# Optimization experiments

Measured on AMD Instinct MI355X. Metric: run time of the kernel, lower is better.

Reference implementation:

```python
import jax, jax.numpy as jnp
import numpy as np

N_NODES = 100000
N_HYPEREDGES = 30000
N_INC = 300000
IN_CH = 128
HID = 256
OUT_CH = 128
EPS = 1e-5


def setup_inputs() -> dict:
    key = jax.random.key(0)
    ks = jax.random.split(key, 14)
    x = jax.random.normal(ks[0], (N_NODES, IN_CH), jnp.float32)
    node_idx = jax.random.randint(ks[1], (N_INC,), 0, N_NODES)
    he_idx = jax.random.randint(ks[2], (N_INC,), 0, N_HYPEREDGES)
    edge = jnp.stack([node_idx, he_idx], axis=0)  # [2, N_INC]
    s1 = 1.0 / np.sqrt(IN_CH)
    s2 = 1.0 / np.sqrt(HID)
    return {
        "x": x,
        "edge": edge,
        "W1": jax.random.normal(ks[3], (IN_CH, HID), jnp.float32) * s1,
        "b1": jnp.zeros((HID,), jnp.float32),
        "g1": jnp.ones((HID,), jnp.float32),
        "be1": jnp.zeros((HID,), jnp.float32),
        "W2": jax.random.normal(ks[4], (HID, HID), jnp.float32) * s2,
        "b2": jnp.zeros((HID,), jnp.float32),
        "g2": jnp.ones((HID,), jnp.float32),
        "be2": jnp.zeros((HID,), jnp.float32),
        "W3": jax.random.normal(ks[5], (HID, OUT_CH), jnp.float32) * s2,
        "b3": jnp.zeros((OUT_CH,), jnp.float32),
    }


def _hconv(x, node_idx, he_idx, W, b):
    # PyG HypergraphConv (no attention, unit hyperedge weights):
    # X' = D^{-1} H B^{-1} H^T (X @ W) + b
    x = x @ W  # [N, F]
    ones = jnp.ones((node_idx.shape[0],), x.dtype)
    d = jax.ops.segment_sum(ones, node_idx, num_segments=N_NODES)       # node degree
    bd = jax.ops.segment_sum(ones, he_idx, num_segments=N_HYPEREDGES)  # hyperedge degree
    Dinv = jnp.where(d > 0, 1.0 / jnp.maximum(d, 1.0), 0.0)
    Binv = jnp.where(bd > 0, 1.0 / jnp.maximum(bd, 1.0), 0.0)
    # node -> hyperedge aggregation, scaled by B^{-1}
    he = jax.ops.segment_sum(x[node_idx], he_idx, num_segments=N_HYPEREDGES) * Binv[:, None]
    # hyperedge -> node aggregation, scaled by D^{-1}
    out = jax.ops.segment_sum(he[he_idx], node_idx, num_segments=N_NODES) * Dinv[:, None]
    return out + b


def _bn(x, g, be):
    # BatchNorm1d, training mode (batch statistics over nodes)
    m = x.mean(axis=0)
    v = x.var(axis=0)
    return (x - m) * jax.lax.rsqrt(v + EPS) * g + be


def reference(x, edge, W1, b1, g1, be1, W2, b2, g2, be2, W3, b3):
    node_idx = edge[0]
    he_idx = edge[1]
    h = _bn(jax.nn.relu(_hconv(x, node_idx, he_idx, W1, b1)), g1, be1)
    h = _bn(jax.nn.relu(_hconv(h, node_idx, he_idx, W2, b2)), g2, be2)
    h = jax.nn.relu(_hconv(h, node_idx, he_idx, W3, b3))
    return h
```

## Files before the change

kernel.cpp:

```cpp
#include <hip/hip_runtime.h>

#define N_NODES 100000
#define N_HE    30000
#define N_INC   300000
#define HEPAD   30080
#define NREP    16

typedef short  short8  __attribute__((ext_vector_type(8)));
typedef float  floatx4 __attribute__((ext_vector_type(4)));
typedef unsigned int uintx4 __attribute__((ext_vector_type(4)));

__device__ inline unsigned short f2bf(float f) {
  unsigned int u = __float_as_uint(f);
  u = (u + 0x7fff + ((u >> 16) & 1)) >> 16;
  return (unsigned short)u;
}
__device__ inline unsigned int pack2(float lo, float hi) {
  return (unsigned int)f2bf(lo) | ((unsigned int)f2bf(hi) << 16);
}
__device__ inline void acc8(uint4 rv, float* a) {
  unsigned int u;
  u = rv.x; a[0] += __uint_as_float(u << 16); a[1] += __uint_as_float(u & 0xffff0000u);
  u = rv.y; a[2] += __uint_as_float(u << 16); a[3] += __uint_as_float(u & 0xffff0000u);
  u = rv.z; a[4] += __uint_as_float(u << 16); a[5] += __uint_as_float(u & 0xffff0000u);
  u = rv.w; a[6] += __uint_as_float(u << 16); a[7] += __uint_as_float(u & 0xffff0000u);
}

struct R4 { uint4 r[4]; };
struct R8 { uint4 r[8]; };

__device__ inline void load4(const unsigned short* __restrict__ base, const int* e,
                             int F, int c0, R4& o) {
#pragma unroll
  for (int k = 0; k < 4; k++)
    o.r[k] = *(const uint4*)(base + (size_t)e[k] * F + c0);
}
__device__ inline void accm4(const R4& o, int d, float* a) {
  if (d > 0) acc8(o.r[0], a);
  if (d > 1) acc8(o.r[1], a);
  if (d > 2) acc8(o.r[2], a);
  if (d > 3) acc8(o.r[3], a);
}
__device__ inline void load8(const unsigned short* __restrict__ base, const int* e,
                             int F, int c0, R8& o) {
#pragma unroll
  for (int k = 0; k < 8; k++)
    o.r[k] = *(const uint4*)(base + (size_t)e[k] * F + c0);
}
__device__ inline void accm8(const R8& o, int d, float* a) {
  acc8(o.r[0], a);
  if (d > 1) acc8(o.r[1], a);
  if (d > 2) acc8(o.r[2], a);
  if (d > 3) acc8(o.r[3], a);
  if (d > 4) acc8(o.r[4], a);
  if (d > 5) acc8(o.r[5], a);
  if (d > 6) acc8(o.r[6], a);
  if (d > 7) acc8(o.r[7], a);
}

__device__ inline void gather8p(const unsigned short* __restrict__ base,
                                const int* __restrict__ idx, int beg, int end,
                                int F, int c0, float* a) {
  if (beg >= end) return;
  int e[8];
#pragma unroll
  for (int k = 0; k < 8; k++) e[k] = idx[min(beg + k, end - 1)];
  for (int j = beg; j < end; j += 8) {
    R8 r;
    load8(base, e, F, c0, r);
    int jn = j + 8;
    if (jn < end) {
#pragma unroll
      for (int k = 0; k < 8; k++) e[k] = idx[min(jn + k, end - 1)];
    }
    accm8(r, end - j, a);
  }
}


__global__ void count_kernel(const int* __restrict__ nidx, const int* __restrict__ hidx,
                             int* __restrict__ node_cnt, int* __restrict__ he_cnt) {
  int i = blockIdx.x * blockDim.x + threadIdx.x;
  if (i < N_INC) {
    atomicAdd(&node_cnt[nidx[i]], 1);
    atomicAdd(&he_cnt[hidx[i]], 1);
  }
}

__global__ void scan1(const int* __restrict__ cnt, int* __restrict__ incl,
                      int* __restrict__ bsums, int n) {
  __shared__ int tmp[1024];
  int tid = threadIdx.x;
  int i = blockIdx.x * 1024 + tid;
  tmp[tid] = (i < n) ? cnt[i] : 0;
  __syncthreads();
  for (int off = 1; off < 1024; off <<= 1) {
    int t = (tid >= off) ? tmp[tid - off] : 0;
    __syncthreads();
    tmp[tid] += t;
    __syncthreads();
  }
  if (i < n) incl[i] = tmp[tid];
  if (tid == 1023) bsums[blockIdx.x] = tmp[1023];
}

__global__ void scan2(int* __restrict__ bsums, int nb) {
  if (threadIdx.x == 0 && blockIdx.x == 0) {
    int run = 0;
    for (int b = 0; b < nb; b++) { int v = bsums[b]; bsums[b] = run; run += v; }
  }
}

__global__ void scan3(const int* __restrict__ cnt, const int* __restrict__ incl,
                      const int* __restrict__ bsums, int* __restrict__ ptr,
                      int* __restrict__ fill, int n) {
  int i = blockIdx.x * 1024 + threadIdx.x;
  if (i < n) {
    int e = incl[i] - cnt[i] + bsums[blockIdx.x];
    ptr[i] = e;
    fill[i] = e;
    if (i == n - 1) ptr[n] = incl[i] + bsums[blockIdx.x];
  }
}

__global__ void fill_kernel(const int* __restrict__ nidx, const int* __restrict__ hidx,
                            int* __restrict__ node_fill, int* __restrict__ he_fill,
                            int* __restrict__ node_hes, int* __restrict__ he_nodes) {
  int i = blockIdx.x * blockDim.x + threadIdx.x;
  if (i < N_INC) {
    int nn = nidx[i], hh = hidx[i];
    int p1 = atomicAdd(&node_fill[nn], 1);
    node_hes[p1] = hh;
    int p2 = atomicAdd(&he_fill[hh], 1);
    he_nodes[p2] = nn;
  }
}


__global__ void convert_x(const float* __restrict__ x, unsigned short* __restrict__ xb) {
  int i = blockIdx.x * 256 + threadIdx.x;
  if (i >= N_NODES * 16) return;
  const float4* p = (const float4*)x + (size_t)i * 2;
  float4 a = p[0], b = p[1];
  uint4 o;
  o.x = pack2(a.x, a.y); o.y = pack2(a.z, a.w);
  o.z = pack2(b.x, b.y); o.w = pack2(b.z, b.w);
  *(uint4*)(xb + (size_t)i * 8) = o;
}

__global__ __launch_bounds__(256) void fold_w(
    const float* __restrict__ W, const float* __restrict__ gsum,
    const float* __restrict__ gss, const float* __restrict__ g,
    const float* __restrict__ be, unsigned short* __restrict__ WT,
    float* __restrict__ cvec, int K, int N, float invN) {
  int n = blockIdx.y * 256 + threadIdx.x;
  if (n >= N) return;
  int k0 = blockIdx.x * 16;
  float c = 0.f;
  unsigned short loc[16];
#pragma unroll
  for (int i = 0; i < 16; i++) {
    int k = k0 + i;
    float w = W[(size_t)k * N + n];
    float s = 1.f, t = 0.f;
    if (gsum) {
      float ms = 0.f, vs = 0.f;
#pragma unroll
      for (int r = 0; r < NREP; r++) { ms += gsum[r * 256 + k]; vs += gss[r * 256 + k]; }
      float m = ms * invN;
      float v = vs * invN - m * m;
      s = g[k] * rsqrtf(v + 1e-5f);
      t = be[k] - m * s;
    }
    loc[i] = f2bf(w * s);
    c += t * w;
  }
  *(uint4*)(WT + (size_t)n * K + k0)     = *(const uint4*)&loc[0];
  *(uint4*)(WT + (size_t)n * K + k0 + 8) = *(const uint4*)&loc[8];
  atomicAdd(cvec + n, c);
}


__global__ __launch_bounds__(256) void gemm_mfma(
    const unsigned short* __restrict__ A, const unsigned short* __restrict__ BT,
    unsigned short* __restrict__ C, int K, int N) {
  __shared__ unsigned short As[128 * 32];
  __shared__ unsigned short Bs[128 * 32];
  const int tid  = threadIdx.x;
  const int w    = tid >> 6, lane = tid & 63;
  const int wm   = w & 1,  wn   = w >> 1;
  const int bm   = blockIdx.x * 128, bn = blockIdx.y * 128;
  const int quad = lane >> 4, r16 = lane & 15;

  floatx4 acc[4][4] = {};

  const int srow = (lane >> 2);
  const int scol = (lane & 3) * 8;

  for (int kb = 0; kb < K; kb += 32) {
#pragma unroll
    for (int i = 0; i < 2; i++) {
      const int row = (w * 2 + i) * 16 + srow;
      const unsigned short* ga = A  + (size_t)(bm + row) * K + kb + scol;
      const unsigned short* gb = BT + (size_t)(bn + row) * K + kb + scol;
      __builtin_amdgcn_global_load_lds(
          (const __attribute__((address_space(1))) void*)ga,
          (__attribute__((address_space(3))) void*)(&As[(w * 2 + i) * 512]), 16, 0, 0);
      __builtin_amdgcn_global_load_lds(
          (const __attribute__((address_space(1))) void*)gb,
          (__attribute__((address_space(3))) void*)(&Bs[(w * 2 + i) * 512]), 16, 0, 0);
    }
    __syncthreads();
    short8 af[4], bfr[4];
#pragma unroll
    for (int t = 0; t < 4; t++) {
      af[t]  = *(const short8*)&As[(wm * 64 + t * 16 + r16) * 32 + quad * 8];
      bfr[t] = *(const short8*)&Bs[(wn * 64 + t * 16 + r16) * 32 + quad * 8];
    }
#pragma unroll
    for (int mi = 0; mi < 4; mi++)
#pragma unroll
      for (int ni = 0; ni < 4; ni++)
        acc[mi][ni] = __builtin_amdgcn_mfma_f32_16x16x32_bf16(af[mi], bfr[ni], acc[mi][ni], 0, 0, 0);
    __syncthreads();
  }
#pragma unroll
  for (int mi = 0; mi < 4; mi++)
#pragma unroll
    for (int ni = 0; ni < 4; ni++)
#pragma unroll
      for (int rr = 0; rr < 4; rr++) {
        int gm = bm + wm * 64 + mi * 16 + quad * 4 + rr;
        int gn = bn + wn * 64 + ni * 16 + r16;
        C[(size_t)gm * N + gn] = f2bf(acc[mi][ni][rr]);
      }
}


__global__ __launch_bounds__(256) void agg_he(
    const unsigned short* __restrict__ src, const int* __restrict__ ptr,
    const int* __restrict__ idx, unsigned short* __restrict__ dst,
    int F, int shift, int nSeg) {
  int seg = blockIdx.x * (256 >> shift) + (threadIdx.x >> shift);
  if (seg >= nSeg) return;
  int l = threadIdx.x & ((1 << shift) - 1);
  int c0 = l * 8;
  int beg = ptr[seg], end = ptr[seg + 1];
  float a[8] = {};
  gather8p(src, idx, beg, end, F, c0, a);
  float inv = (end > beg) ? 1.0f / (float)(end - beg) : 0.0f;
  uint4 o;
  o.x = pack2(a[0] * inv, a[1] * inv);
  o.y = pack2(a[2] * inv, a[3] * inv);
  o.z = pack2(a[4] * inv, a[5] * inv);
  o.w = pack2(a[6] * inv, a[7] * inv);
  *(uint4*)(dst + (size_t)seg * F + c0) = o;
}

__global__ __launch_bounds__(256) void node_agg_bn(
    const unsigned short* __restrict__ he, const int* __restrict__ nptr,
    const int* __restrict__ nhes, const float* __restrict__ b,
    const float* __restrict__ cvec, unsigned short* __restrict__ dst,
    float* __restrict__ gsum, float* __restrict__ gss) {
  const int F = 256;
  const int grp = threadIdx.x >> 5, l = threadIdx.x & 31, c0 = l * 8;
  float bb[8], cc[8];
#pragma unroll
  for (int j = 0; j < 8; j++) { bb[j] = b[c0 + j]; cc[j] = cvec[c0 + j]; }
  int begs[8], ends[8];
#pragma unroll
  for (int i = 0; i < 8; i++) {
    int n = blockIdx.x * 64 + i * 8 + grp;
    begs[i] = (n < N_NODES) ? nptr[n] : 0;
    ends[i] = (n < N_NODES) ? nptr[n + 1] : 0;
  }
  int e[8][4];
#pragma unroll
  for (int i = 0; i < 8; i++) {
    int bg = begs[i], en = ends[i];
#pragma unroll
    for (int k = 0; k < 4; k++)
      e[i][k] = (bg < en) ? nhes[min(bg + k, en - 1)] : 0;
  }
  float s[8] = {}, ss[8] = {};
#pragma unroll
  for (int q = 0; q < 2; q++) {
    R4 r0, r1, r2, r3;
    load4(he, e[q * 4 + 0], F, c0, r0);
    load4(he, e[q * 4 + 1], F, c0, r1);
    load4(he, e[q * 4 + 2], F, c0, r2);
    load4(he, e[q * 4 + 3], F, c0, r3);
#pragma unroll
    for (int t = 0; t < 4; t++) {
      const int i = q * 4 + t;
      const int d = ends[i] - begs[i];
      float a[8] = {};
      const R4& rr = (t == 0) ? r0 : (t == 1) ? r1 : (t == 2) ? r2 : r3;
      accm4(rr, d, a);
      for (int j = begs[i] + 4; j < ends[i]; j += 4) {
        int et[4];
#pragma unroll
        for (int k = 0; k < 4; k++) et[k] = nhes[min(j + k, ends[i] - 1)];
        R4 tt; load4(he, et, F, c0, tt);
        accm4(tt, ends[i] - j, a);
      }
      const int n = blockIdx.x * 64 + i * 8 + grp;
      if (n < N_NODES) {
        float inv  = (d > 0) ? 1.0f / (float)d : 0.0f;
        float cmul = (d > 0) ? 1.0f : 0.0f;
        float o[8];
#pragma unroll
        for (int j = 0; j < 8; j++) {
          o[j] = fmaxf(fmaf(a[j], inv, bb[j] + cmul * cc[j]), 0.f);
          s[j] += o[j]; ss[j] += o[j] * o[j];
        }
        uintx4 ov;
        ov.x = pack2(o[0], o[1]); ov.y = pack2(o[2], o[3]);
        ov.z = pack2(o[4], o[5]); ov.w = pack2(o[6], o[7]);
        __builtin_nontemporal_store(ov, (uintx4*)(dst + (size_t)n * F + c0));
      }
    }
  }
  __shared__ float Ls[8][256];
  __shared__ float Lss[8][256];
#pragma unroll
  for (int j = 0; j < 8; j++) { Ls[grp][c0 + j] = s[j]; Lss[grp][c0 + j] = ss[j]; }
  __syncthreads();
  int c = threadIdx.x;
  float a1 = 0.f, a2 = 0.f;
#pragma unroll
  for (int h = 0; h < 8; h++) { a1 += Ls[h][c]; a2 += Lss[h][c]; }
  const int rep = blockIdx.x & (NREP - 1);
  atomicAdd(gsum + rep * 256 + c, a1);
  atomicAdd(gss  + rep * 256 + c, a2);
}

__global__ __launch_bounds__(256) void agg_out(
    const unsigned short* __restrict__ he, const int* __restrict__ nptr,
    const int* __restrict__ nhes, const float* __restrict__ b,
    const float* __restrict__ cvec, float* __restrict__ out) {
  const int F = 128;
  int g = threadIdx.x >> 4, l = threadIdx.x & 15, c0 = l * 8;
  int nA = blockIdx.x * 32 + g, nB = nA + 16;
  int begA = (nA < N_NODES) ? nptr[nA] : 0;
  int endA = (nA < N_NODES) ? nptr[nA + 1] : 0;
  int begB = (nB < N_NODES) ? nptr[nB] : 0;
  int endB = (nB < N_NODES) ? nptr[nB + 1] : 0;
  int dA = endA - begA, dB = endB - begB;
  int eA[4], eB[4];
#pragma unroll
  for (int k = 0; k < 4; k++) {
    eA[k] = (dA > 0) ? nhes[min(begA + k, endA - 1)] : 0;
    eB[k] = (dB > 0) ? nhes[min(begB + k, endB - 1)] : 0;
  }
  R4 rA, rB;
  load4(he, eA, F, c0, rA);
  load4(he, eB, F, c0, rB);
  float aA[8] = {}, aB[8] = {};
  accm4(rA, dA, aA);
  for (int j = begA + 4; j < endA; j += 4) {
    int et[4];
#pragma unroll
    for (int k = 0; k < 4; k++) et[k] = nhes[min(j + k, endA - 1)];
    R4 t; load4(he, et, F, c0, t);
    accm4(t, endA - j, aA);
  }
  accm4(rB, dB, aB);
  for (int j = begB + 4; j < endB; j += 4) {
    int et[4];
#pragma unroll
    for (int k = 0; k < 4; k++) et[k] = nhes[min(j + k, endB - 1)];
    R4 t; load4(he, et, F, c0, t);
    accm4(t, endB - j, aB);
  }
#pragma unroll
  for (int q = 0; q < 2; q++) {
    int n = q ? nB : nA;
    if (n >= N_NODES) continue;
    int d = q ? dB : dA;
    const float* a = q ? aB : aA;
    float inv  = (d > 0) ? 1.0f / (float)d : 0.0f;
    float cmul = (d > 0) ? 1.0f : 0.0f;
    floatx4 o0, o1;
    o0[0] = fmaxf(fmaf(a[0], inv, b[c0 + 0] + cmul * cvec[c0 + 0]), 0.f);
    o0[1] = fmaxf(fmaf(a[1], inv, b[c0 + 1] + cmul * cvec[c0 + 1]), 0.f);
    o0[2] = fmaxf(fmaf(a[2], inv, b[c0 + 2] + cmul * cvec[c0 + 2]), 0.f);
    o0[3] = fmaxf(fmaf(a[3], inv, b[c0 + 3] + cmul * cvec[c0 + 3]), 0.f);
    o1[0] = fmaxf(fmaf(a[4], inv, b[c0 + 4] + cmul * cvec[c0 + 4]), 0.f);
    o1[1] = fmaxf(fmaf(a[5], inv, b[c0 + 5] + cmul * cvec[c0 + 5]), 0.f);
    o1[2] = fmaxf(fmaf(a[6], inv, b[c0 + 6] + cmul * cvec[c0 + 6]), 0.f);
    o1[3] = fmaxf(fmaf(a[7], inv, b[c0 + 7] + cmul * cvec[c0 + 7]), 0.f);
    float* dp = out + (size_t)n * F + c0;
    __builtin_nontemporal_store(o0, (floatx4*)dp);
    __builtin_nontemporal_store(o1, (floatx4*)(dp + 4));
  }
}


extern "C" void kernel_launch(void* const* d_in, const int* in_sizes, int n_in,
                              void* d_out, int out_size, void* d_ws, size_t ws_size,
                              hipStream_t stream) {
  const float* x    = (const float*)d_in[0];
  const int*   edge = (const int*)d_in[1];
  const int*   nidx = edge;
  const int*   hidx = edge + N_INC;
  const float* W1  = (const float*)d_in[2];
  const float* b1  = (const float*)d_in[3];
  const float* g1  = (const float*)d_in[4];
  const float* be1 = (const float*)d_in[5];
  const float* W2  = (const float*)d_in[6];
  const float* b2  = (const float*)d_in[7];
  const float* g2  = (const float*)d_in[8];
  const float* be2 = (const float*)d_in[9];
  const float* W3  = (const float*)d_in[10];
  const float* b3  = (const float*)d_in[11];
  float* out = (float*)d_out;

  char* ws = (char*)d_ws;
  size_t off = 0;
  auto alloc = [&](size_t bytes) -> void* {
    void* p = ws + off;
    off = (off + bytes + 255) & ~(size_t)255;
    return p;
  };
  unsigned short* Xb   = (unsigned short*)alloc((size_t)N_NODES * 128 * 2);
  unsigned short* Bb   = (unsigned short*)alloc((size_t)N_NODES * 256 * 2);
  unsigned short* Hraw = (unsigned short*)alloc((size_t)HEPAD * 256 * 2);
  unsigned short* HEb  = (unsigned short*)alloc((size_t)HEPAD * 256 * 2);
  unsigned short* W1T  = (unsigned short*)alloc((size_t)256 * 128 * 2);
  unsigned short* W2T  = (unsigned short*)alloc((size_t)256 * 256 * 2);
  unsigned short* W3T  = (unsigned short*)alloc((size_t)128 * 256 * 2);
  size_t zero_begin = off;
  int* he_cnt   = (int*)alloc((size_t)N_HE * 4);
  int* node_cnt = (int*)alloc((size_t)N_NODES * 4);
  float* gsum1 = (float*)alloc((size_t)NREP * 256 * 4);
  float* gss1  = (float*)alloc((size_t)NREP * 256 * 4);
  float* gsum2 = (float*)alloc((size_t)NREP * 256 * 4);
  float* gss2  = (float*)alloc((size_t)NREP * 256 * 4);
  float* c1 = (float*)alloc(1024);
  float* c2 = (float*)alloc(1024);
  float* c3 = (float*)alloc(1024);
  size_t zero_end = off;
  int* he_ptr    = (int*)alloc((size_t)(N_HE + 1) * 4);
  int* node_ptr  = (int*)alloc((size_t)(N_NODES + 1) * 4);
  int* he_fill   = (int*)alloc((size_t)N_HE * 4);
  int* node_fill = (int*)alloc((size_t)N_NODES * 4);
  int* he_nodes  = (int*)alloc((size_t)N_INC * 4);
  int* node_hes  = (int*)alloc((size_t)N_INC * 4);
  int* incl      = (int*)alloc((size_t)N_NODES * 4);
  int* bsums     = (int*)alloc(512);

  hipMemsetAsync((void*)(ws + zero_begin), 0, zero_end - zero_begin, stream);

  count_kernel<<<(N_INC + 255) / 256, 256, 0, stream>>>(nidx, hidx, node_cnt, he_cnt);
  {
    int nb = (N_HE + 1023) / 1024;
    scan1<<<nb, 1024, 0, stream>>>(he_cnt, incl, bsums, N_HE);
    scan2<<<1, 64, 0, stream>>>(bsums, nb);
    scan3<<<nb, 1024, 0, stream>>>(he_cnt, incl, bsums, he_ptr, he_fill, N_HE);
  }
  {
    int nb = (N_NODES + 1023) / 1024;
    scan1<<<nb, 1024, 0, stream>>>(node_cnt, incl, bsums, N_NODES);
    scan2<<<1, 64, 0, stream>>>(bsums, nb);
    scan3<<<nb, 1024, 0, stream>>>(node_cnt, incl, bsums, node_ptr, node_fill, N_NODES);
  }
  fill_kernel<<<(N_INC + 255) / 256, 256, 0, stream>>>(nidx, hidx, node_fill, he_fill,
                                                       node_hes, he_nodes);

  convert_x<<<(N_NODES * 16 + 255) / 256, 256, 0, stream>>>(x, Xb);
  { dim3 g(128 / 16, 1);
    fold_w<<<g, 256, 0, stream>>>(W1, nullptr, nullptr, nullptr, nullptr, W1T, c1, 128, 256, 0.f); }

  const int MBHE = HEPAD / 128;
  const float invN = 1.0f / (float)N_NODES;

  agg_he<<<(N_HE + 15) / 16, 256, 0, stream>>>(Xb, he_ptr, he_nodes, Hraw, 128, 4, N_HE);
  { dim3 g(MBHE, 2); gemm_mfma<<<g, 256, 0, stream>>>(Hraw, W1T, HEb, 128, 256); }
  node_agg_bn<<<(N_NODES + 63) / 64, 256, 0, stream>>>(HEb, node_ptr, node_hes, b1, c1,
                                                       Bb, gsum1, gss1);

  { dim3 g(256 / 16, 1);
    fold_w<<<g, 256, 0, stream>>>(W2, gsum1, gss1, g1, be1, W2T, c2, 256, 256, invN); }
  agg_he<<<(N_HE + 7) / 8, 256, 0, stream>>>(Bb, he_ptr, he_nodes, Hraw, 256, 5, N_HE);
  { dim3 g(MBHE, 2); gemm_mfma<<<g, 256, 0, stream>>>(Hraw, W2T, HEb, 256, 256); }
  node_agg_bn<<<(N_NODES + 63) / 64, 256, 0, stream>>>(HEb, node_ptr, node_hes, b2, c2,
                                                       Bb, gsum2, gss2);

  { dim3 g(256 / 16, 1);
    fold_w<<<g, 256, 0, stream>>>(W3, gsum2, gss2, g2, be2, W3T, c3, 256, 128, invN); }
  agg_he<<<(N_HE + 7) / 8, 256, 0, stream>>>(Bb, he_ptr, he_nodes, Hraw, 256, 5, N_HE);
  { dim3 g(MBHE, 1); gemm_mfma<<<g, 256, 0, stream>>>(Hraw, W3T, HEb, 256, 128); }
  agg_out<<<(N_NODES + 31) / 32, 256, 0, stream>>>(HEb, node_ptr, node_hes, b3, c3, out);
}
```

Measured before the change: 434.6 us.

## Split node aggregation by column slices and parallelize block-sum scan

The node-side aggregation kernels (node_agg_bn and agg_out) now split the feature dimension into 64-column slices across separate blocks. Each block handles 128 nodes with 8 lanes per node row instead of 32 or 16. This shrinks the gathered working set per block (a 64-column slice of HE) so it may stay resident in cache, and it raises the number of blocks. The cost is re-reading the CSR pointers and indices once per slice, plus smaller 16-byte-per-lane row segments. The single-threaded scan2 is also replaced with a 128-thread shared-memory parallel scan.

```diff
diff --git a/kernel.cpp b/kernel.cpp
--- a/kernel.cpp
+++ b/kernel.cpp
@@ -105,10 +105,18 @@
 }
 
 __global__ void scan2(int* __restrict__ bsums, int nb) {
-  if (threadIdx.x == 0 && blockIdx.x == 0) {
-    int run = 0;
-    for (int b = 0; b < nb; b++) { int v = bsums[b]; bsums[b] = run; run += v; }
-  }
+  __shared__ int tmp[128];
+  int t = threadIdx.x;
+  int my = (t < nb) ? bsums[t] : 0;
+  tmp[t] = my;
+  __syncthreads();
+  for (int off = 1; off < 128; off <<= 1) {
+    int v = (t >= off) ? tmp[t - off] : 0;
+    __syncthreads();
+    tmp[t] += v;
+    __syncthreads();
+  }
+  if (t < nb) bsums[t] = tmp[t] - my;
 }
 
 __global__ void scan3(const int* __restrict__ cnt, const int* __restrict__ incl,
@@ -261,138 +269,143 @@
     const unsigned short* __restrict__ he, const int* __restrict__ nptr,
     const int* __restrict__ nhes, const float* __restrict__ b,
     const float* __restrict__ cvec, unsigned short* __restrict__ dst,
-    float* __restrict__ gsum, float* __restrict__ gss) {
+    float* __restrict__ gsum, float* __restrict__ gss, int qblks) {
   const int F = 256;
-  const int grp = threadIdx.x >> 5, l = threadIdx.x & 31, c0 = l * 8;
+  const int qi = blockIdx.x / qblks;
+  const int xb = blockIdx.x % qblks;
+  const int grp = threadIdx.x >> 3;
+  const int l   = threadIdx.x & 7;
+  const int c0  = qi * 64 + l * 8;
   float bb[8], cc[8];
 #pragma unroll
   for (int j = 0; j < 8; j++) { bb[j] = b[c0 + j]; cc[j] = cvec[c0 + j]; }
-  int begs[8], ends[8];
-#pragma unroll
-  for (int i = 0; i < 8; i++) {
-    int n = blockIdx.x * 64 + i * 8 + grp;
+  const int base_n = xb * 128 + grp * 4;
+  int begs[4], ends[4];
+#pragma unroll
+  for (int i = 0; i < 4; i++) {
+    int n = base_n + i;
     begs[i] = (n < N_NODES) ? nptr[n] : 0;
     ends[i] = (n < N_NODES) ? nptr[n + 1] : 0;
   }
-  int e[8][4];
-#pragma unroll
-  for (int i = 0; i < 8; i++) {
-    int bg = begs[i], en = ends[i];
+  int e[4][4];
+#pragma unroll
+  for (int i = 0; i < 4; i++) {
 #pragma unroll
     for (int k = 0; k < 4; k++)
-      e[i][k] = (bg < en) ? nhes[min(bg + k, en - 1)] : 0;
-  }
-  float s[8] = {}, ss[8] = {};
-#pragma unroll
-  for (int q = 0; q < 2; q++) {
-    R4 r0, r1, r2, r3;
-    load4(he, e[q * 4 + 0], F, c0, r0);
-    load4(he, e[q * 4 + 1], F, c0, r1);
-    load4(he, e[q * 4 + 2], F, c0, r2);
-    load4(he, e[q * 4 + 3], F, c0, r3);
-#pragma unroll
-    for (int t = 0; t < 4; t++) {
-      const int i = q * 4 + t;
-      const int d = ends[i] - begs[i];
-      float a[8] = {};
-      const R4& rr = (t == 0) ? r0 : (t == 1) ? r1 : (t == 2) ? r2 : r3;
-      accm4(rr, d, a);
-      for (int j = begs[i] + 4; j < ends[i]; j += 4) {
-        int et[4];
-#pragma unroll
-        for (int k = 0; k < 4; k++) et[k] = nhes[min(j + k, ends[i] - 1)];
-        R4 tt; load4(he, et, F, c0, tt);
-        accm4(tt, ends[i] - j, a);
+      e[i][k] = (begs[i] < ends[i]) ? nhes[min(begs[i] + k, ends[i] - 1)] : 0;
+  }
+  R4 r0, r1, r2, r3;
+  load4(he, e[0], F, c0, r0);
+  load4(he, e[1], F, c0, r1);
+  load4(he, e[2], F, c0, r2);
+  load4(he, e[3], F, c0, r3);
+  float sb[8] = {}, ssb[8] = {};
+#pragma unroll
+  for (int t = 0; t < 4; t++) {
+    const int d = ends[t] - begs[t];
+    float a[8] = {};
+    const R4& rr = (t == 0) ? r0 : (t == 1) ? r1 : (t == 2) ? r2 : r3;
+    accm4(rr, d, a);
+    for (int j = begs[t] + 4; j < ends[t]; j += 4) {
+      int et[4];
+#pragma unroll
+      for (int k = 0; k < 4; k++) et[k] = nhes[min(j + k, ends[t] - 1)];
+      R4 tt; load4(he, et, F, c0, tt);
+      accm4(tt, ends[t] - j, a);
+    }
+    const int n = base_n + t;
+    if (n < N_NODES) {
+      float inv  = (d > 0) ? 1.0f / (float)d : 0.0f;
+      float cmul = (d > 0) ? 1.0f : 0.0f;
+      float o[8];
+#pragma unroll
+      for (int j = 0; j < 8; j++) {
+        o[j] = fmaxf(fmaf(a[j], inv, bb[j] + cmul * cc[j]), 0.f);
+        sb[j] += o[j]; ssb[j] += o[j] * o[j];
       }
-      const int n = blockIdx.x * 64 + i * 8 + grp;
-      if (n < N_NODES) {
-        float inv  = (d > 0) ? 1.0f / (float)d : 0.0f;
-        float cmul = (d > 0) ? 1.0f : 0.0f;
-        float o[8];
-#pragma unroll
-        for (int j = 0; j < 8; j++) {
-          o[j] = fmaxf(fmaf(a[j], inv, bb[j] + cmul * cc[j]), 0.f);
-          s[j] += o[j]; ss[j] += o[j] * o[j];
-        }
-        uintx4 ov;
-        ov.x = pack2(o[0], o[1]); ov.y = pack2(o[2], o[3]);
-        ov.z = pack2(o[4], o[5]); ov.w = pack2(o[6], o[7]);
-        __builtin_nontemporal_store(ov, (uintx4*)(dst + (size_t)n * F + c0));
-      }
-    }
-  }
-  __shared__ float Ls[8][256];
-  __shared__ float Lss[8][256];
-#pragma unroll
-  for (int j = 0; j < 8; j++) { Ls[grp][c0 + j] = s[j]; Lss[grp][c0 + j] = ss[j]; }
+      uintx4 ov;
+      ov.x = pack2(o[0], o[1]); ov.y = pack2(o[2], o[3]);
+      ov.z = pack2(o[4], o[5]); ov.w = pack2(o[6], o[7]);
+      __builtin_nontemporal_store(ov, (uintx4*)(dst + (size_t)n * F + c0));
+    }
+  }
+  __shared__ float Ls[32][64];
+  __shared__ float Lss[32][64];
+#pragma unroll
+  for (int j = 0; j < 8; j++) { Ls[grp][l * 8 + j] = sb[j]; Lss[grp][l * 8 + j] = ssb[j]; }
   __syncthreads();
-  int c = threadIdx.x;
-  float a1 = 0.f, a2 = 0.f;
-#pragma unroll
-  for (int h = 0; h < 8; h++) { a1 += Ls[h][c]; a2 += Lss[h][c]; }
-  const int rep = blockIdx.x & (NREP - 1);
-  atomicAdd(gsum + rep * 256 + c, a1);
-  atomicAdd(gss  + rep * 256 + c, a2);
+  if (threadIdx.x < 64) {
+    int c = threadIdx.x;
+    float a1 = 0.f, a2 = 0.f;
+#pragma unroll
+    for (int h = 0; h < 32; h++) { a1 += Ls[h][c]; a2 += Lss[h][c]; }
+    const int rep = xb & (NREP - 1);
+    atomicAdd(gsum + rep * 256 + qi * 64 + c, a1);
+    atomicAdd(gss  + rep * 256 + qi * 64 + c, a2);
+  }
 }
 
 __global__ __launch_bounds__(256) void agg_out(
     const unsigned short* __restrict__ he, const int* __restrict__ nptr,
     const int* __restrict__ nhes, const float* __restrict__ b,
-    const float* __restrict__ cvec, float* __restrict__ out) {
+    const float* __restrict__ cvec, float* __restrict__ out, int oblks) {
   const int F = 128;
-  int g = threadIdx.x >> 4, l = threadIdx.x & 15, c0 = l * 8;
-  int nA = blockIdx.x * 32 + g, nB = nA + 16;
-  int begA = (nA < N_NODES) ? nptr[nA] : 0;
-  int endA = (nA < N_NODES) ? nptr[nA + 1] : 0;
-  int begB = (nB < N_NODES) ? nptr[nB] : 0;
-  int endB = (nB < N_NODES) ? nptr[nB + 1] : 0;
-  int dA = endA - begA, dB = endB - begB;
-  int eA[4], eB[4];
-#pragma unroll
-  for (int k = 0; k < 4; k++) {
-    eA[k] = (dA > 0) ? nhes[min(begA + k, endA - 1)] : 0;
-    eB[k] = (dB > 0) ? nhes[min(begB + k, endB - 1)] : 0;
-  }
-  R4 rA, rB;
-  load4(he, eA, F, c0, rA);
-  load4(he, eB, F, c0, rB);
-  float aA[8] = {}, aB[8] = {};
-  accm4(rA, dA, aA);
-  for (int j = begA + 4; j < endA; j += 4) {
-    int et[4];
-#pragma unroll
-    for (int k = 0; k < 4; k++) et[k] = nhes[min(j + k, endA - 1)];
-    R4 t; load4(he, et, F, c0, t);
-    accm4(t, endA - j, aA);
-  }
-  accm4(rB, dB, aB);
-  for (int j = begB + 4; j < endB; j += 4) {
-    int et[4];
-#pragma unroll
-    for (int k = 0; k < 4; k++) et[k] = nhes[min(j + k, endB - 1)];
-    R4 t; load4(he, et, F, c0, t);
-    accm4(t, endB - j, aB);
-  }
-#pragma unroll
-  for (int q = 0; q < 2; q++) {
-    int n = q ? nB : nA;
-    if (n >= N_NODES) continue;
-    int d = q ? dB : dA;
-    const float* a = q ? aB : aA;
-    float inv  = (d > 0) ? 1.0f / (float)d : 0.0f;
-    float cmul = (d > 0) ? 1.0f : 0.0f;
-    floatx4 o0, o1;
-    o0[0] = fmaxf(fmaf(a[0], inv, b[c0 + 0] + cmul * cvec[c0 + 0]), 0.f);
-    o0[1] = fmaxf(fmaf(a[1], inv, b[c0 + 1] + cmul * cvec[c0 + 1]), 0.f);
-    o0[2] = fmaxf(fmaf(a[2], inv, b[c0 + 2] + cmul * cvec[c0 + 2]), 0.f);
-    o0[3] = fmaxf(fmaf(a[3], inv, b[c0 + 3] + cmul * cvec[c0 + 3]), 0.f);
-    o1[0] = fmaxf(fmaf(a[4], inv, b[c0 + 4] + cmul * cvec[c0 + 4]), 0.f);
-    o1[1] = fmaxf(fmaf(a[5], inv, b[c0 + 5] + cmul * cvec[c0 + 5]), 0.f);
-    o1[2] = fmaxf(fmaf(a[6], inv, b[c0 + 6] + cmul * cvec[c0 + 6]), 0.f);
-    o1[3] = fmaxf(fmaf(a[7], inv, b[c0 + 7] + cmul * cvec[c0 + 7]), 0.f);
-    float* dp = out + (size_t)n * F + c0;
-    __builtin_nontemporal_store(o0, (floatx4*)dp);
-    __builtin_nontemporal_store(o1, (floatx4*)(dp + 4));
+  const int hi = blockIdx.x / oblks;
+  const int xb = blockIdx.x % oblks;
+  const int grp = threadIdx.x >> 3;
+  const int l   = threadIdx.x & 7;
+  const int c0  = hi * 64 + l * 8;
+  float bb[8], cc[8];
+#pragma unroll
+  for (int j = 0; j < 8; j++) { bb[j] = b[c0 + j]; cc[j] = cvec[c0 + j]; }
+  const int base_n = xb * 128 + grp * 4;
+  int begs[4], ends[4];
+#pragma unroll
+  for (int i = 0; i < 4; i++) {
+    int n = base_n + i;
+    begs[i] = (n < N_NODES) ? nptr[n] : 0;
+    ends[i] = (n < N_NODES) ? nptr[n + 1] : 0;
+  }
+  int e[4][4];
+#pragma unroll
+  for (int i = 0; i < 4; i++) {
+#pragma unroll
+    for (int k = 0; k < 4; k++)
+      e[i][k] = (begs[i] < ends[i]) ? nhes[min(begs[i] + k, ends[i] - 1)] : 0;
+  }
+  R4 r0, r1, r2, r3;
+  load4(he, e[0], F, c0, r0);
+  load4(he, e[1], F, c0, r1);
+  load4(he, e[2], F, c0, r2);
+  load4(he, e[3], F, c0, r3);
+#pragma unroll
+  for (int t = 0; t < 4; t++) {
+    const int d = ends[t] - begs[t];
+    float a[8] = {};
+    const R4& rr = (t == 0) ? r0 : (t == 1) ? r1 : (t == 2) ? r2 : r3;
+    accm4(rr, d, a);
+    for (int j = begs[t] + 4; j < ends[t]; j += 4) {
+      int et[4];
+#pragma unroll
+      for (int k = 0; k < 4; k++) et[k] = nhes[min(j + k, ends[t] - 1)];
+      R4 tt; load4(he, et, F, c0, tt);
+      accm4(tt, ends[t] - j, a);
+    }
+    const int n = base_n + t;
+    if (n < N_NODES) {
+      float inv  = (d > 0) ? 1.0f / (float)d : 0.0f;
+      float cmul = (d > 0) ? 1.0f : 0.0f;
+      floatx4 o0, o1;
+#pragma unroll
+      for (int j = 0; j < 4; j++)
+        o0[j] = fmaxf(fmaf(a[j], inv, bb[j] + cmul * cc[j]), 0.f);
+#pragma unroll
+      for (int j = 0; j < 4; j++)
+        o1[j] = fmaxf(fmaf(a[4 + j], inv, bb[4 + j] + cmul * cc[4 + j]), 0.f);
+      float* dp = out + (size_t)n * F + c0;
+      __builtin_nontemporal_store(o0, (floatx4*)dp);
+      __builtin_nontemporal_store(o1, (floatx4*)(dp + 4));
+    }
   }
 }
 
@@ -456,13 +469,13 @@
   {
     int nb = (N_HE + 1023) / 1024;
     scan1<<<nb, 1024, 0, stream>>>(he_cnt, incl, bsums, N_HE);
-    scan2<<<1, 64, 0, stream>>>(bsums, nb);
+    scan2<<<1, 128, 0, stream>>>(bsums, nb);
     scan3<<<nb, 1024, 0, stream>>>(he_cnt, incl, bsums, he_ptr, he_fill, N_HE);
   }
   {
     int nb = (N_NODES + 1023) / 1024;
     scan1<<<nb, 1024, 0, stream>>>(node_cnt, incl, bsums, N_NODES);
-    scan2<<<1, 64, 0, stream>>>(bsums, nb);
+    scan2<<<1, 128, 0, stream>>>(bsums, nb);
     scan3<<<nb, 1024, 0, stream>>>(node_cnt, incl, bsums, node_ptr, node_fill, N_NODES);
   }
   fill_kernel<<<(N_INC + 255) / 256, 256, 0, stream>>>(nidx, hidx, node_fill, he_fill,
@@ -473,23 +486,24 @@
     fold_w<<<g, 256, 0, stream>>>(W1, nullptr, nullptr, nullptr, nullptr, W1T, c1, 128, 256, 0.f); }
 
   const int MBHE = HEPAD / 128;
+  const int QB = (N_NODES + 127) / 128;
   const float invN = 1.0f / (float)N_NODES;
 
   agg_he<<<(N_HE + 15) / 16, 256, 0, stream>>>(Xb, he_ptr, he_nodes, Hraw, 128, 4, N_HE);
   { dim3 g(MBHE, 2); gemm_mfma<<<g, 256, 0, stream>>>(Hraw, W1T, HEb, 128, 256); }
-  node_agg_bn<<<(N_NODES + 63) / 64, 256, 0, stream>>>(HEb, node_ptr, node_hes, b1, c1,
-                                                       Bb, gsum1, gss1);
+  node_agg_bn<<<QB * 4, 256, 0, stream>>>(HEb, node_ptr, node_hes, b1, c1,
+                                          Bb, gsum1, gss1, QB);
 
   { dim3 g(256 / 16, 1);
     fold_w<<<g, 256, 0, stream>>>(W2, gsum1, gss1, g1, be1, W2T, c2, 256, 256, invN); }
   agg_he<<<(N_HE + 7) / 8, 256, 0, stream>>>(Bb, he_ptr, he_nodes, Hraw, 256, 5, N_HE);
   { dim3 g(MBHE, 2); gemm_mfma<<<g, 256, 0, stream>>>(Hraw, W2T, HEb, 256, 256); }
-  node_agg_bn<<<(N_NODES + 63) / 64, 256, 0, stream>>>(HEb, node_ptr, node_hes, b2, c2,
-                                                       Bb, gsum2, gss2);
+  node_agg_bn<<<QB * 4, 256, 0, stream>>>(HEb, node_ptr, node_hes, b2, c2,
+                                          Bb, gsum2, gss2, QB);
 
   { dim3 g(256 / 16, 1);
     fold_w<<<g, 256, 0, stream>>>(W3, gsum2, gss2, g2, be2, W3T, c3, 256, 128, invN); }
   agg_he<<<(N_HE + 7) / 8, 256, 0, stream>>>(Bb, he_ptr, he_nodes, Hraw, 256, 5, N_HE);
   { dim3 g(MBHE, 1); gemm_mfma<<<g, 256, 0, stream>>>(Hraw, W3T, HEb, 256, 128); }
-  agg_out<<<(N_NODES + 31) / 32, 256, 0, stream>>>(HEb, node_ptr, node_hes, b3, c3, out);
-}
+  agg_out<<<QB * 2, 256, 0, stream>>>(HEb, node_ptr, node_hes, b3, c3, out, QB);
+}
```

After: 424.4 us. -2.3%, faster.
